# Kernel optimization log

Measured on AMD Instinct MI355X. Metric: run time of the kernel, lower is better.

## Reference

```python
import jax, jax.numpy as jnp
import numpy as np

N = 50000       # nodes
E = 800000      # edges (avg degree 16)
D_IN = 128      # input_dim
HID = 128       # hidden_dim
G_FEAT = 32     # g_feat_dim
G = 64          # number of graphs in batch
EPS = 1e-5      # BatchNorm eps


def _lin_init(key, fan_in, fan_out):
    s = 1.0 / np.sqrt(fan_in)
    return jax.random.uniform(key, (fan_in, fan_out), jnp.float32, -s, s)


def setup_inputs() -> dict:
    key = jax.random.key(0)
    ks = jax.random.split(key, 24)
    inp = {
        'x': jax.random.normal(ks[0], (N, D_IN), jnp.float32),
        'edge_index': jax.random.randint(ks[1], (2, E), 0, N, jnp.int64),
        'batch': jnp.sort(jax.random.randint(ks[2], (N,), 0, G, jnp.int64)),
        'g_feats': jax.random.normal(ks[3], (G, G_FEAT), jnp.float32),
    }
    dims = [D_IN, HID, HID]
    k = 4
    for i, din in enumerate(dims):
        inp[f'Wl{i}'] = _lin_init(ks[k], din, HID); k += 1   # lin_l (neighbors, has bias)
        inp[f'bl{i}'] = jnp.zeros((HID,), jnp.float32)
        inp[f'Wr{i}'] = _lin_init(ks[k], din, HID); k += 1   # lin_r (self, no bias in PyG)
        inp[f'gamma{i}'] = jnp.ones((HID,), jnp.float32)
        inp[f'beta{i}'] = jnp.zeros((HID,), jnp.float32)
    inp['W1'] = _lin_init(ks[k], 2 * HID + G_FEAT, HID); k += 1
    inp['b1'] = jnp.zeros((HID,), jnp.float32)
    inp['W2'] = _lin_init(ks[k], HID, HID // 2); k += 1
    inp['b2'] = jnp.zeros((HID // 2,), jnp.float32)
    inp['W3'] = _lin_init(ks[k], HID // 2, 1); k += 1
    inp['b3'] = jnp.zeros((1,), jnp.float32)
    return inp


def _sage_conv(h, src, dst, Wl, bl, Wr):
    # mean-aggregate neighbor messages x_j into target i, then lin_l(agg)+lin_r(self)
    msgs = h[src]  # [E, d] irregular gather
    agg = jax.ops.segment_sum(msgs, dst, num_segments=N)
    cnt = jax.ops.segment_sum(jnp.ones((E,), h.dtype), dst, num_segments=N)
    agg = agg / jnp.clip(cnt, 1.0)[:, None]
    return agg @ Wl + bl + h @ Wr


def _batch_norm(h, gamma, beta):
    mu = jnp.mean(h, axis=0)
    var = jnp.var(h, axis=0)
    return gamma * (h - mu) * jax.lax.rsqrt(var + EPS) + beta


def _forward(x, edge_index, batch, g_feats, convs, head):
    src, dst = edge_index[0], edge_index[1]
    h = x
    for (Wl, bl, Wr, gamma, beta) in convs:
        h = jax.nn.relu(_batch_norm(_sage_conv(h, src, dst, Wl, bl, Wr), gamma, beta))
        # dropout p=0.01: identity in eval/reference mode
    cnt = jnp.clip(jax.ops.segment_sum(jnp.ones((N,), h.dtype), batch, num_segments=G), 1.0)
    hg_mean = jax.ops.segment_sum(h, batch, num_segments=G) / cnt[:, None]
    hg_max = jax.ops.segment_max(h, batch, num_segments=G)
    W1, b1, W2, b2, W3, b3 = head
    m = jnp.concatenate([hg_mean, hg_max, g_feats], axis=1)  # [G, 2*HID+G_FEAT]
    m = jax.nn.relu(m @ W1 + b1)
    m = jax.nn.relu(m @ W2 + b2)
    return (m @ W3 + b3).reshape(-1)  # [G]


def reference(x, edge_index, batch, g_feats,
              Wl0, bl0, Wr0, gamma0, beta0,
              Wl1, bl1, Wr1, gamma1, beta1,
              Wl2, bl2, Wr2, gamma2, beta2,
              W1, b1, W2, b2, W3, b3):
    convs = [(Wl0, bl0, Wr0, gamma0, beta0),
             (Wl1, bl1, Wr1, gamma1, beta1),
             (Wl2, bl2, Wr2, gamma2, beta2)]
    head = (W1, b1, W2, b2, W3, b3)
    return _forward(x, edge_index, batch, g_feats, convs, head)
```

## Files before the change

### kernel.cpp

```cpp
#include <hip/hip_runtime.h>
#include <stdint.h>

#define NN 50000
#define NE 800000
#define HID 128
#define NG 64
#define BN_EPS 1e-5f
#define SC_NB 8
#define SC_BSZ ((NN + SC_NB - 1) / SC_NB)
#define SC_CHUNK 4096
#define SC_CHUNKS ((NE + SC_CHUNK - 1) / SC_CHUNK)
#define CAP 96
#define LAYER_BLOCKS (NN / 16)
#define NPART 64

typedef __bf16 bf16x8 __attribute__((ext_vector_type(8)));
typedef float floatx4 __attribute__((ext_vector_type(4)));

__device__ __forceinline__ float b2f(unsigned short u) {
    union { unsigned int i; float f; } x; x.i = ((unsigned int)u) << 16; return x.f;
}
__device__ __forceinline__ float blo(unsigned int d) { return __uint_as_float(d << 16); }
__device__ __forceinline__ float bhi(unsigned int d) { return __uint_as_float(d & 0xffff0000u); }
__device__ __forceinline__ unsigned short f2b(float f) {
    union { float f; unsigned int i; } x; x.f = f; unsigned int i = x.i;
    if ((i & 0x7f800000u) == 0x7f800000u) return (unsigned short)(i >> 16);
    return (unsigned short)((i + 0x7fffu + ((i >> 16) & 1u)) >> 16);
}
__device__ __forceinline__ unsigned int pack2(float f0, float f1) {
    return (((unsigned int)f2b(f1)) << 16) | f2b(f0);
}
__device__ __forceinline__ float2 bn_pair_part(const float* __restrict__ part,
                                               const float* __restrict__ gamma,
                                               const float* __restrict__ beta, int c) {
    float s = 0.f, sq = 0.f;
#pragma unroll 8
    for (int k = 0; k < NPART; ++k) {
        s += part[k * 256 + c];
        sq += part[k * 256 + 128 + c];
    }
    float mu = s * (1.f / NN);
    float var = sq * (1.f / NN) - mu * mu;
    float sc = gamma[c] * rsqrtf(var + BN_EPS);
    return make_float2(sc, beta[c] - mu * sc);
}
__device__ __forceinline__ int lbound(const int* __restrict__ batch, int val) {
    int lo = 0, hi = NN;
    while (lo < hi) { int mid = (lo + hi) >> 1; if (batch[mid] < val) lo = mid + 1; else hi = mid; }
    return lo;
}

__global__ void k_setup(const float* __restrict__ x, unsigned short* xb, int* cnt,
                        float* part, float* pool_sum, int* pool_max,
                        const float* __restrict__ Wl0, const float* __restrict__ Wr0,
                        const float* __restrict__ Wl1, const float* __restrict__ Wr1,
                        const float* __restrict__ Wl2, const float* __restrict__ Wr2,
                        unsigned short* Bp) {
    int i = blockIdx.x * 256 + threadIdx.x;
    if (i < NN * 64) {
        float2 v = ((const float2*)x)[i];
        ((unsigned int*)xb)[i] = pack2(v.x, v.y);
    }
    if (i < NN) cnt[i] = 0;
    if (i < 3 * NPART * 256) part[i] = 0.f;
    if (i < NG * HID) { pool_sum[i] = 0.f; pool_max[i] = 0; }
    if (i < 3 * 32768) {
        int layer = i >> 15;
        int r = i & 32767;
        int nt = r >> 12, kk = (r >> 9) & 7, l = (r >> 3) & 63, j = r & 7;
        int k = kk * 32 + (l >> 4) * 8 + j;
        int n = nt * 16 + (l & 15);
        const float* Wl = layer == 0 ? Wl0 : (layer == 1 ? Wl1 : Wl2);
        const float* Wr = layer == 0 ? Wr0 : (layer == 1 ? Wr1 : Wr2);
        Bp[i] = f2b((k < 128) ? Wl[k * 128 + n] : Wr[(k - 128) * 128 + n]);
    }
}

__global__ void k_scatter(const int* __restrict__ src, const int* __restrict__ dst,
                          int* cnt, int* col) {
    int bucket = blockIdx.x & (SC_NB - 1);
    int chunk = blockIdx.x / SC_NB;
    int lo = bucket * SC_BSZ, hi = lo + SC_BSZ;
    int base = chunk * SC_CHUNK;
#pragma unroll
    for (int i = 0; i < SC_CHUNK / 256; ++i) {
        int e = base + i * 256 + threadIdx.x;
        if (e < NE) {
            int d = dst[e];
            if (d >= lo && d < hi) {
                int p = atomicAdd(&cnt[d], 1);
                if (p < CAP) col[d * CAP + p] = src[e];
            }
        }
    }
}

__global__ void __launch_bounds__(256) k_layer(const unsigned short* __restrict__ h,
                                               const int* __restrict__ cnt,
                                               const int* __restrict__ col,
                                               const unsigned short* __restrict__ Bg,
                                               float* __restrict__ part,
                                               unsigned short* __restrict__ out) {
    __shared__ uint4 aggt4[256];
    __shared__ uint4 selft4[256];
    int t = threadIdx.x;
    int wid = t >> 6, lane = t & 63;
    const uint4* h4 = (const uint4*)h;
    {
        int slot = lane >> 4, sub = lane & 15;
        int nl = wid * 4 + slot;
        int node = blockIdx.x * 16 + nl;
        int n = cnt[node]; if (n > CAP) n = CAP;
        const int* row = col + (size_t)node * CAP;
        uint4 sv = h4[(size_t)node * 16 + sub];
        float a0 = 0.f, a1 = 0.f, a2 = 0.f, a3 = 0.f, a4 = 0.f, a5 = 0.f, a6 = 0.f, a7 = 0.f;
        int j = 0;
        for (; j + 8 <= n; j += 8) {
            int u0 = row[j], u1 = row[j + 1], u2 = row[j + 2], u3 = row[j + 3];
            int u4 = row[j + 4], u5 = row[j + 5], u6 = row[j + 6], u7 = row[j + 7];
            uint4 v0 = h4[(size_t)u0 * 16 + sub];
            uint4 v1 = h4[(size_t)u1 * 16 + sub];
            uint4 v2 = h4[(size_t)u2 * 16 + sub];
            uint4 v3 = h4[(size_t)u3 * 16 + sub];
            uint4 v4 = h4[(size_t)u4 * 16 + sub];
            uint4 v5 = h4[(size_t)u5 * 16 + sub];
            uint4 v6 = h4[(size_t)u6 * 16 + sub];
            uint4 v7 = h4[(size_t)u7 * 16 + sub];
            a0 += ((blo(v0.x) + blo(v1.x)) + (blo(v2.x) + blo(v3.x))) +
                  ((blo(v4.x) + blo(v5.x)) + (blo(v6.x) + blo(v7.x)));
            a1 += ((bhi(v0.x) + bhi(v1.x)) + (bhi(v2.x) + bhi(v3.x))) +
                  ((bhi(v4.x) + bhi(v5.x)) + (bhi(v6.x) + bhi(v7.x)));
            a2 += ((blo(v0.y) + blo(v1.y)) + (blo(v2.y) + blo(v3.y))) +
                  ((blo(v4.y) + blo(v5.y)) + (blo(v6.y) + blo(v7.y)));
            a3 += ((bhi(v0.y) + bhi(v1.y)) + (bhi(v2.y) + bhi(v3.y))) +
                  ((bhi(v4.y) + bhi(v5.y)) + (bhi(v6.y) + bhi(v7.y)));
            a4 += ((blo(v0.z) + blo(v1.z)) + (blo(v2.z) + blo(v3.z))) +
                  ((blo(v4.z) + blo(v5.z)) + (blo(v6.z) + blo(v7.z)));
            a5 += ((bhi(v0.z) + bhi(v1.z)) + (bhi(v2.z) + bhi(v3.z))) +
                  ((bhi(v4.z) + bhi(v5.z)) + (bhi(v6.z) + bhi(v7.z)));
            a6 += ((blo(v0.w) + blo(v1.w)) + (blo(v2.w) + blo(v3.w))) +
                  ((blo(v4.w) + blo(v5.w)) + (blo(v6.w) + blo(v7.w)));
            a7 += ((bhi(v0.w) + bhi(v1.w)) + (bhi(v2.w) + bhi(v3.w))) +
                  ((bhi(v4.w) + bhi(v5.w)) + (bhi(v6.w) + bhi(v7.w)));
        }
        for (; j + 4 <= n; j += 4) {
            int u0 = row[j], u1 = row[j + 1], u2 = row[j + 2], u3 = row[j + 3];
            uint4 v0 = h4[(size_t)u0 * 16 + sub];
            uint4 v1 = h4[(size_t)u1 * 16 + sub];
            uint4 v2 = h4[(size_t)u2 * 16 + sub];
            uint4 v3 = h4[(size_t)u3 * 16 + sub];
            a0 += (blo(v0.x) + blo(v1.x)) + (blo(v2.x) + blo(v3.x));
            a1 += (bhi(v0.x) + bhi(v1.x)) + (bhi(v2.x) + bhi(v3.x));
            a2 += (blo(v0.y) + blo(v1.y)) + (blo(v2.y) + blo(v3.y));
            a3 += (bhi(v0.y) + bhi(v1.y)) + (bhi(v2.y) + bhi(v3.y));
            a4 += (blo(v0.z) + blo(v1.z)) + (blo(v2.z) + blo(v3.z));
            a5 += (bhi(v0.z) + bhi(v1.z)) + (bhi(v2.z) + bhi(v3.z));
            a6 += (blo(v0.w) + blo(v1.w)) + (blo(v2.w) + blo(v3.w));
            a7 += (bhi(v0.w) + bhi(v1.w)) + (bhi(v2.w) + bhi(v3.w));
        }
        for (; j < n; ++j) {
            int u = row[j];
            uint4 v = h4[(size_t)u * 16 + sub];
            a0 += blo(v.x);  a1 += bhi(v.x);
            a2 += blo(v.y);  a3 += bhi(v.y);
            a4 += blo(v.z);  a5 += bhi(v.z);
            a6 += blo(v.w);  a7 += bhi(v.w);
        }
        float inv = (n > 0) ? 1.f / (float)n : 0.f;
        uint4 o;
        o.x = pack2(a0 * inv, a1 * inv);
        o.y = pack2(a2 * inv, a3 * inv);
        o.z = pack2(a4 * inv, a5 * inv);
        o.w = pack2(a6 * inv, a7 * inv);
        int swz = sub ^ (nl & 7);
        aggt4[nl * 16 + swz] = o;
        selft4[nl * 16 + swz] = sv;
    }
    __syncthreads();
    int m = lane & 15, q = lane >> 4;
    int mbase = blockIdx.x * 16;
    const bf16x8* Bv = (const bf16x8*)Bg;
    bf16x8 af[8];
#pragma unroll
    for (int kk = 0; kk < 4; ++kk) {
        int ci = (kk * 4 + q) ^ (m & 7);
        af[kk] = *(const bf16x8*)&aggt4[m * 16 + ci];
        af[4 + kk] = *(const bf16x8*)&selft4[m * 16 + ci];
    }
    floatx4 acc[2];
    acc[0] = (floatx4){0.f, 0.f, 0.f, 0.f};
    acc[1] = (floatx4){0.f, 0.f, 0.f, 0.f};
#pragma unroll
    for (int kk = 0; kk < 8; ++kk) {
#pragma unroll
        for (int ntl = 0; ntl < 2; ++ntl) {
            int nt = wid * 2 + ntl;
            bf16x8 b = Bv[(nt * 8 + kk) * 64 + lane];
            acc[ntl] = __builtin_amdgcn_mfma_f32_16x16x32_bf16(af[kk], b, acc[ntl], 0, 0, 0);
        }
    }
    float s8[2] = {0.f, 0.f}, ss8[2] = {0.f, 0.f};
#pragma unroll
    for (int ntl = 0; ntl < 2; ++ntl) {
        int c = (wid * 2 + ntl) * 16 + m;
#pragma unroll
        for (int reg = 0; reg < 4; ++reg) {
            int r = mbase + q * 4 + reg;
            float v = acc[ntl][reg];
            out[(size_t)r * 128 + c] = f2b(v);
            s8[ntl] += v;
            ss8[ntl] += v * v;
        }
        s8[ntl] += __shfl_xor(s8[ntl], 16, 64);  s8[ntl] += __shfl_xor(s8[ntl], 32, 64);
        ss8[ntl] += __shfl_xor(ss8[ntl], 16, 64); ss8[ntl] += __shfl_xor(ss8[ntl], 32, 64);
    }
    float* pb = part + (blockIdx.x & (NPART - 1)) * 256;
    if (lane < 16) {
#pragma unroll
        for (int ntl = 0; ntl < 2; ++ntl) {
            int c = (wid * 2 + ntl) * 16 + m;
            atomicAdd(&pb[c], s8[ntl]);
            atomicAdd(&pb[128 + c], ss8[ntl]);
        }
    }
}

__global__ void k_norm(const unsigned short* __restrict__ pre,
                       const float* __restrict__ part, const float* __restrict__ gamma,
                       const float* __restrict__ beta, unsigned short* __restrict__ hn) {
    __shared__ float sc[128], sh[128];
    int t = threadIdx.x;
    if (t < 128) {
        float2 p = bn_pair_part(part, gamma, beta, t);
        sc[t] = p.x; sh[t] = p.y;
    }
    __syncthreads();
#pragma unroll
    for (int ii = 0; ii < 4; ++ii) {
        int i = (blockIdx.x * 4 + ii) * 256 + t;
        if (i < NN * 16) {
            uint4 v = ((const uint4*)pre)[i];
            int cb = (i & 15) * 8;
            uint4 o;
            o.x = pack2(fmaxf(blo(v.x) * sc[cb + 0] + sh[cb + 0], 0.f),
                        fmaxf(bhi(v.x) * sc[cb + 1] + sh[cb + 1], 0.f));
            o.y = pack2(fmaxf(blo(v.y) * sc[cb + 2] + sh[cb + 2], 0.f),
                        fmaxf(bhi(v.y) * sc[cb + 3] + sh[cb + 3], 0.f));
            o.z = pack2(fmaxf(blo(v.z) * sc[cb + 4] + sh[cb + 4], 0.f),
                        fmaxf(bhi(v.z) * sc[cb + 5] + sh[cb + 5], 0.f));
            o.w = pack2(fmaxf(blo(v.w) * sc[cb + 6] + sh[cb + 6], 0.f),
                        fmaxf(bhi(v.w) * sc[cb + 7] + sh[cb + 7], 0.f));
            ((uint4*)hn)[i] = o;
        }
    }
}

__global__ void k_pool(const unsigned short* __restrict__ h, const int* __restrict__ batch,
                       const float* __restrict__ part,
                       const float* __restrict__ gamma, const float* __restrict__ beta,
                       float* pool_sum, int* pool_max) {
    int g = blockIdx.x >> 3, chunk = blockIdx.x & 7;
    int s = lbound(batch, g), e1 = lbound(batch, g + 1);
    if (s >= e1) return;
    int cnt = e1 - s;
    int per = (cnt + 7) >> 3;
    int r0 = s + chunk * per;
    int r1 = min(r0 + per, e1);
    int c = threadIdx.x & 127, half = threadIdx.x >> 7;
    float2 pr = bn_pair_part(part, gamma, beta, c);
    float sm = 0.f, mx = 0.f;
    for (int r = r0 + half; r < r1; r += 2) {
        float v = fmaxf(b2f(h[(size_t)r * 128 + c]) * pr.x + pr.y, 0.f);
        sm += v;
        mx = fmaxf(mx, v);
    }
    atomicAdd(&pool_sum[g * 128 + c], sm);
    atomicMax(&pool_max[g * 128 + c], __float_as_int(mx));
}

__global__ void __launch_bounds__(128) k_head(
    const float* __restrict__ pool_sum, const int* __restrict__ pool_max,
    const int* __restrict__ batch, const float* __restrict__ gfeats,
    const float* __restrict__ W1, const float* __restrict__ bs1,
    const float* __restrict__ W2, const float* __restrict__ bs2,
    const float* __restrict__ W3, const float* __restrict__ bs3,
    float* out) {
    __shared__ float m[288];
    __shared__ float o1[128];
    __shared__ float o2[64];
    int g = blockIdx.x, t = threadIdx.x;
    int cint = lbound(batch, g + 1) - lbound(batch, g);
    float cnt = (float)(cint < 1 ? 1 : cint);
    if (t < 128) {
        m[t] = pool_sum[g * 128 + t] / cnt;
        m[128 + t] = __int_as_float(pool_max[g * 128 + t]);
    }
    if (t < 32) m[256 + t] = gfeats[g * 32 + t];
    __syncthreads();
    float acc = bs1[t];
    for (int k = 0; k < 288; ++k) acc += m[k] * W1[k * 128 + t];
    o1[t] = fmaxf(acc, 0.f);
    __syncthreads();
    if (t < 64) {
        float a2 = bs2[t];
        for (int k = 0; k < 128; ++k) a2 += o1[k] * W2[k * 64 + t];
        o2[t] = fmaxf(a2, 0.f);
    }
    __syncthreads();
    if (t < 64) {
        float p = o2[t] * W3[t];
#pragma unroll
        for (int off = 32; off; off >>= 1) p += __shfl_down(p, off, 64);
        if (t == 0) out[g] = p + bs3[0];
    }
}

extern "C" void kernel_launch(void* const* d_in, const int* in_sizes, int n_in,
                              void* d_out, int out_size, void* d_ws, size_t ws_size,
                              hipStream_t stream) {
    const float* x = (const float*)d_in[0];
    const int* ei = (const int*)d_in[1];
    const int* batch = (const int*)d_in[2];
    const float* gfeats = (const float*)d_in[3];
    const float *Wl[3], *Wr[3], *gma[3], *bta[3];
    for (int i = 0; i < 3; ++i) {
        Wl[i] = (const float*)d_in[4 + 5 * i];
        Wr[i] = (const float*)d_in[6 + 5 * i];
        gma[i] = (const float*)d_in[7 + 5 * i];
        bta[i] = (const float*)d_in[8 + 5 * i];
    }
    const float* W1 = (const float*)d_in[19];
    const float* bs1 = (const float*)d_in[20];
    const float* W2 = (const float*)d_in[21];
    const float* bs2 = (const float*)d_in[22];
    const float* W3 = (const float*)d_in[23];
    const float* bs3 = (const float*)d_in[24];

    char* p = (char*)d_ws;
    auto alloc = [&](size_t bytes) -> char* {
        char* r = p;
        p += (bytes + 255) & ~(size_t)255;
        return r;
    };
    int* cnt = (int*)alloc(NN * 4);
    int* col = (int*)alloc((size_t)NN * CAP * 4);
    float* part = (float*)alloc(3 * NPART * 256 * 4);
    float* pool_sum = (float*)alloc(NG * HID * 4);
    int* pool_max = (int*)alloc(NG * HID * 4);
    unsigned short* Bp = (unsigned short*)alloc(3 * 32768 * 2);
    unsigned short* xb = (unsigned short*)alloc((size_t)NN * 128 * 2);
    unsigned short* b0 = (unsigned short*)alloc((size_t)NN * 128 * 2);
    unsigned short* b1 = (unsigned short*)alloc((size_t)NN * 128 * 2);
    unsigned short* hn0 = (unsigned short*)alloc((size_t)NN * 128 * 2);

    const int* srcv = ei;
    const int* dstv = ei + NE;

    k_setup<<<(NN * 64 + 255) / 256, 256, 0, stream>>>(
        x, xb, cnt, part, pool_sum, pool_max,
        Wl[0], Wr[0], Wl[1], Wr[1], Wl[2], Wr[2], Bp);
    k_scatter<<<SC_CHUNKS * SC_NB, 256, 0, stream>>>(srcv, dstv, cnt, col);

    k_layer<<<LAYER_BLOCKS, 256, 0, stream>>>(xb, cnt, col, Bp, part, b0);
    k_norm<<<(NN * 16 + 1023) / 1024, 256, 0, stream>>>(b0, part, gma[0], bta[0], hn0);
    k_layer<<<LAYER_BLOCKS, 256, 0, stream>>>(hn0, cnt, col, Bp + 32768, part + 16384, b1);
    k_norm<<<(NN * 16 + 1023) / 1024, 256, 0, stream>>>(b1, part + 16384, gma[1], bta[1], xb);
    k_layer<<<LAYER_BLOCKS, 256, 0, stream>>>(xb, cnt, col, Bp + 65536, part + 32768, b0);

    k_pool<<<NG * 8, 256, 0, stream>>>(b0, batch, part + 32768, gma[2], bta[2],
                                       pool_sum, pool_max);
    k_head<<<NG, 128, 0, stream>>>(pool_sum, pool_max, batch, gfeats,
                                   W1, bs1, W2, bs2, W3, bs3, (float*)d_out);
}
```

Measured before the change: 332.1 us.

## Split per-node edge counters by parity and fuse pooling with MLP head

The edge scatter now spreads atomics across two counters per destination node, chosen by edge parity, each with its own half of the neighbor slots. This is meant to cut contention on the per-node atomic counters. The pooling and head kernels are merged into one launch: the last block to finish, detected with a global done counter, runs the MLP head for all graphs. This removes one kernel launch but runs the whole head serially in a single block, and a node whose edges fall unevenly across the two halves now overflows at 48 slots per half instead of 96 total.

```diff
diff --git a/kernel.cpp b/kernel.cpp
--- a/kernel.cpp
+++ b/kernel.cpp
@@ -11,6 +11,7 @@
 #define SC_CHUNK 4096
 #define SC_CHUNKS ((NE + SC_CHUNK - 1) / SC_CHUNK)
 #define CAP 96
+#define SUBCAP 48
 #define LAYER_BLOCKS (NN / 16)
 #define NPART 64
 
@@ -50,8 +51,8 @@
     return lo;
 }
 
-__global__ void k_setup(const float* __restrict__ x, unsigned short* xb, int* cnt,
-                        float* part, float* pool_sum, int* pool_max,
+__global__ void k_setup(const float* __restrict__ x, unsigned short* xb, int* cnt2,
+                        float* part, float* pool_sum, int* pool_max, int* done,
                         const float* __restrict__ Wl0, const float* __restrict__ Wr0,
                         const float* __restrict__ Wl1, const float* __restrict__ Wr1,
                         const float* __restrict__ Wl2, const float* __restrict__ Wr2,
@@ -61,7 +62,8 @@
         float2 v = ((const float2*)x)[i];
         ((unsigned int*)xb)[i] = pack2(v.x, v.y);
     }
-    if (i < NN) cnt[i] = 0;
+    if (i < NN * 2) cnt2[i] = 0;
+    if (i == 0) done[0] = 0;
     if (i < 3 * NPART * 256) part[i] = 0.f;
     if (i < NG * HID) { pool_sum[i] = 0.f; pool_max[i] = 0; }
     if (i < 3 * 32768) {
@@ -77,7 +79,7 @@
 }
 
 __global__ void k_scatter(const int* __restrict__ src, const int* __restrict__ dst,
-                          int* cnt, int* col) {
+                          int* cnt2, int* col) {
     int bucket = blockIdx.x & (SC_NB - 1);
     int chunk = blockIdx.x / SC_NB;
     int lo = bucket * SC_BSZ, hi = lo + SC_BSZ;
@@ -88,15 +90,16 @@
         if (e < NE) {
             int d = dst[e];
             if (d >= lo && d < hi) {
-                int p = atomicAdd(&cnt[d], 1);
-                if (p < CAP) col[d * CAP + p] = src[e];
+                int s = e & 1;
+                int p = atomicAdd(&cnt2[d * 2 + s], 1);
+                if (p < SUBCAP) col[d * CAP + s * SUBCAP + p] = src[e];
             }
         }
     }
 }
 
 __global__ void __launch_bounds__(256) k_layer(const unsigned short* __restrict__ h,
-                                               const int* __restrict__ cnt,
+                                               const int* __restrict__ cnt2,
                                                const int* __restrict__ col,
                                                const unsigned short* __restrict__ Bg,
                                                float* __restrict__ part,
@@ -110,62 +113,69 @@
         int slot = lane >> 4, sub = lane & 15;
         int nl = wid * 4 + slot;
         int node = blockIdx.x * 16 + nl;
-        int n = cnt[node]; if (n > CAP) n = CAP;
+        int2 c2 = ((const int2*)cnt2)[node];
+        int n0 = min(c2.x, SUBCAP), n1 = min(c2.y, SUBCAP);
         const int* row = col + (size_t)node * CAP;
         uint4 sv = h4[(size_t)node * 16 + sub];
         float a0 = 0.f, a1 = 0.f, a2 = 0.f, a3 = 0.f, a4 = 0.f, a5 = 0.f, a6 = 0.f, a7 = 0.f;
-        int j = 0;
-        for (; j + 8 <= n; j += 8) {
-            int u0 = row[j], u1 = row[j + 1], u2 = row[j + 2], u3 = row[j + 3];
-            int u4 = row[j + 4], u5 = row[j + 5], u6 = row[j + 6], u7 = row[j + 7];
-            uint4 v0 = h4[(size_t)u0 * 16 + sub];
-            uint4 v1 = h4[(size_t)u1 * 16 + sub];
-            uint4 v2 = h4[(size_t)u2 * 16 + sub];
-            uint4 v3 = h4[(size_t)u3 * 16 + sub];
-            uint4 v4 = h4[(size_t)u4 * 16 + sub];
-            uint4 v5 = h4[(size_t)u5 * 16 + sub];
-            uint4 v6 = h4[(size_t)u6 * 16 + sub];
-            uint4 v7 = h4[(size_t)u7 * 16 + sub];
-            a0 += ((blo(v0.x) + blo(v1.x)) + (blo(v2.x) + blo(v3.x))) +
-                  ((blo(v4.x) + blo(v5.x)) + (blo(v6.x) + blo(v7.x)));
-            a1 += ((bhi(v0.x) + bhi(v1.x)) + (bhi(v2.x) + bhi(v3.x))) +
-                  ((bhi(v4.x) + bhi(v5.x)) + (bhi(v6.x) + bhi(v7.x)));
-            a2 += ((blo(v0.y) + blo(v1.y)) + (blo(v2.y) + blo(v3.y))) +
-                  ((blo(v4.y) + blo(v5.y)) + (blo(v6.y) + blo(v7.y)));
-            a3 += ((bhi(v0.y) + bhi(v1.y)) + (bhi(v2.y) + bhi(v3.y))) +
-                  ((bhi(v4.y) + bhi(v5.y)) + (bhi(v6.y) + bhi(v7.y)));
-            a4 += ((blo(v0.z) + blo(v1.z)) + (blo(v2.z) + blo(v3.z))) +
-                  ((blo(v4.z) + blo(v5.z)) + (blo(v6.z) + blo(v7.z)));
-            a5 += ((bhi(v0.z) + bhi(v1.z)) + (bhi(v2.z) + bhi(v3.z))) +
-                  ((bhi(v4.z) + bhi(v5.z)) + (bhi(v6.z) + bhi(v7.z)));
-            a6 += ((blo(v0.w) + blo(v1.w)) + (blo(v2.w) + blo(v3.w))) +
-                  ((blo(v4.w) + blo(v5.w)) + (blo(v6.w) + blo(v7.w)));
-            a7 += ((bhi(v0.w) + bhi(v1.w)) + (bhi(v2.w) + bhi(v3.w))) +
-                  ((bhi(v4.w) + bhi(v5.w)) + (bhi(v6.w) + bhi(v7.w)));
-        }
-        for (; j + 4 <= n; j += 4) {
-            int u0 = row[j], u1 = row[j + 1], u2 = row[j + 2], u3 = row[j + 3];
-            uint4 v0 = h4[(size_t)u0 * 16 + sub];
-            uint4 v1 = h4[(size_t)u1 * 16 + sub];
-            uint4 v2 = h4[(size_t)u2 * 16 + sub];
-            uint4 v3 = h4[(size_t)u3 * 16 + sub];
-            a0 += (blo(v0.x) + blo(v1.x)) + (blo(v2.x) + blo(v3.x));
-            a1 += (bhi(v0.x) + bhi(v1.x)) + (bhi(v2.x) + bhi(v3.x));
-            a2 += (blo(v0.y) + blo(v1.y)) + (blo(v2.y) + blo(v3.y));
-            a3 += (bhi(v0.y) + bhi(v1.y)) + (bhi(v2.y) + bhi(v3.y));
-            a4 += (blo(v0.z) + blo(v1.z)) + (blo(v2.z) + blo(v3.z));
-            a5 += (bhi(v0.z) + bhi(v1.z)) + (bhi(v2.z) + bhi(v3.z));
-            a6 += (blo(v0.w) + blo(v1.w)) + (blo(v2.w) + blo(v3.w));
-            a7 += (bhi(v0.w) + bhi(v1.w)) + (bhi(v2.w) + bhi(v3.w));
-        }
-        for (; j < n; ++j) {
-            int u = row[j];
-            uint4 v = h4[(size_t)u * 16 + sub];
-            a0 += blo(v.x);  a1 += bhi(v.x);
-            a2 += blo(v.y);  a3 += bhi(v.y);
-            a4 += blo(v.z);  a5 += bhi(v.z);
-            a6 += blo(v.w);  a7 += bhi(v.w);
-        }
+#pragma unroll
+        for (int sseg = 0; sseg < 2; ++sseg) {
+            int n = sseg ? n1 : n0;
+            const int* rw = row + sseg * SUBCAP;
+            int j = 0;
+            for (; j + 8 <= n; j += 8) {
+                int u0 = rw[j], u1 = rw[j + 1], u2 = rw[j + 2], u3 = rw[j + 3];
+                int u4 = rw[j + 4], u5 = rw[j + 5], u6 = rw[j + 6], u7 = rw[j + 7];
+                uint4 v0 = h4[(size_t)u0 * 16 + sub];
+                uint4 v1 = h4[(size_t)u1 * 16 + sub];
+                uint4 v2 = h4[(size_t)u2 * 16 + sub];
+                uint4 v3 = h4[(size_t)u3 * 16 + sub];
+                uint4 v4 = h4[(size_t)u4 * 16 + sub];
+                uint4 v5 = h4[(size_t)u5 * 16 + sub];
+                uint4 v6 = h4[(size_t)u6 * 16 + sub];
+                uint4 v7 = h4[(size_t)u7 * 16 + sub];
+                a0 += ((blo(v0.x) + blo(v1.x)) + (blo(v2.x) + blo(v3.x))) +
+                      ((blo(v4.x) + blo(v5.x)) + (blo(v6.x) + blo(v7.x)));
+                a1 += ((bhi(v0.x) + bhi(v1.x)) + (bhi(v2.x) + bhi(v3.x))) +
+                      ((bhi(v4.x) + bhi(v5.x)) + (bhi(v6.x) + bhi(v7.x)));
+                a2 += ((blo(v0.y) + blo(v1.y)) + (blo(v2.y) + blo(v3.y))) +
+                      ((blo(v4.y) + blo(v5.y)) + (blo(v6.y) + blo(v7.y)));
+                a3 += ((bhi(v0.y) + bhi(v1.y)) + (bhi(v2.y) + bhi(v3.y))) +
+                      ((bhi(v4.y) + bhi(v5.y)) + (bhi(v6.y) + bhi(v7.y)));
+                a4 += ((blo(v0.z) + blo(v1.z)) + (blo(v2.z) + blo(v3.z))) +
+                      ((blo(v4.z) + blo(v5.z)) + (blo(v6.z) + blo(v7.z)));
+                a5 += ((bhi(v0.z) + bhi(v1.z)) + (bhi(v2.z) + bhi(v3.z))) +
+                      ((bhi(v4.z) + bhi(v5.z)) + (bhi(v6.z) + bhi(v7.z)));
+                a6 += ((blo(v0.w) + blo(v1.w)) + (blo(v2.w) + blo(v3.w))) +
+                      ((blo(v4.w) + blo(v5.w)) + (blo(v6.w) + blo(v7.w)));
+                a7 += ((bhi(v0.w) + bhi(v1.w)) + (bhi(v2.w) + bhi(v3.w))) +
+                      ((bhi(v4.w) + bhi(v5.w)) + (bhi(v6.w) + bhi(v7.w)));
+            }
+            for (; j + 4 <= n; j += 4) {
+                int u0 = rw[j], u1 = rw[j + 1], u2 = rw[j + 2], u3 = rw[j + 3];
+                uint4 v0 = h4[(size_t)u0 * 16 + sub];
+                uint4 v1 = h4[(size_t)u1 * 16 + sub];
+                uint4 v2 = h4[(size_t)u2 * 16 + sub];
+                uint4 v3 = h4[(size_t)u3 * 16 + sub];
+                a0 += (blo(v0.x) + blo(v1.x)) + (blo(v2.x) + blo(v3.x));
+                a1 += (bhi(v0.x) + bhi(v1.x)) + (bhi(v2.x) + bhi(v3.x));
+                a2 += (blo(v0.y) + blo(v1.y)) + (blo(v2.y) + blo(v3.y));
+                a3 += (bhi(v0.y) + bhi(v1.y)) + (bhi(v2.y) + bhi(v3.y));
+                a4 += (blo(v0.z) + blo(v1.z)) + (blo(v2.z) + blo(v3.z));
+                a5 += (bhi(v0.z) + bhi(v1.z)) + (bhi(v2.z) + bhi(v3.z));
+                a6 += (blo(v0.w) + blo(v1.w)) + (blo(v2.w) + blo(v3.w));
+                a7 += (bhi(v0.w) + bhi(v1.w)) + (bhi(v2.w) + bhi(v3.w));
+            }
+            for (; j < n; ++j) {
+                int u = rw[j];
+                uint4 v = h4[(size_t)u * 16 + sub];
+                a0 += blo(v.x);  a1 += bhi(v.x);
+                a2 += blo(v.y);  a3 += bhi(v.y);
+                a4 += blo(v.z);  a5 += bhi(v.z);
+                a6 += blo(v.w);  a7 += bhi(v.w);
+            }
+        }
+        int n = n0 + n1;
         float inv = (n > 0) ? 1.f / (float)n : 0.f;
         uint4 o;
         o.x = pack2(a0 * inv, a1 * inv);
@@ -255,63 +265,72 @@
     }
 }
 
-__global__ void k_pool(const unsigned short* __restrict__ h, const int* __restrict__ batch,
-                       const float* __restrict__ part,
-                       const float* __restrict__ gamma, const float* __restrict__ beta,
-                       float* pool_sum, int* pool_max) {
-    int g = blockIdx.x >> 3, chunk = blockIdx.x & 7;
-    int s = lbound(batch, g), e1 = lbound(batch, g + 1);
-    if (s >= e1) return;
-    int cnt = e1 - s;
-    int per = (cnt + 7) >> 3;
-    int r0 = s + chunk * per;
-    int r1 = min(r0 + per, e1);
-    int c = threadIdx.x & 127, half = threadIdx.x >> 7;
-    float2 pr = bn_pair_part(part, gamma, beta, c);
-    float sm = 0.f, mx = 0.f;
-    for (int r = r0 + half; r < r1; r += 2) {
-        float v = fmaxf(b2f(h[(size_t)r * 128 + c]) * pr.x + pr.y, 0.f);
-        sm += v;
-        mx = fmaxf(mx, v);
-    }
-    atomicAdd(&pool_sum[g * 128 + c], sm);
-    atomicMax(&pool_max[g * 128 + c], __float_as_int(mx));
-}
-
-__global__ void __launch_bounds__(128) k_head(
-    const float* __restrict__ pool_sum, const int* __restrict__ pool_max,
-    const int* __restrict__ batch, const float* __restrict__ gfeats,
+__global__ void __launch_bounds__(256) k_pool_head(
+    const unsigned short* __restrict__ h, const int* __restrict__ batch,
+    const float* __restrict__ part,
+    const float* __restrict__ gamma, const float* __restrict__ beta,
+    float* pool_sum, int* pool_max, int* done,
+    const float* __restrict__ gfeats,
     const float* __restrict__ W1, const float* __restrict__ bs1,
     const float* __restrict__ W2, const float* __restrict__ bs2,
     const float* __restrict__ W3, const float* __restrict__ bs3,
     float* out) {
-    __shared__ float m[288];
-    __shared__ float o1[128];
-    __shared__ float o2[64];
-    int g = blockIdx.x, t = threadIdx.x;
-    int cint = lbound(batch, g + 1) - lbound(batch, g);
-    float cnt = (float)(cint < 1 ? 1 : cint);
-    if (t < 128) {
-        m[t] = pool_sum[g * 128 + t] / cnt;
-        m[128 + t] = __int_as_float(pool_max[g * 128 + t]);
-    }
-    if (t < 32) m[256 + t] = gfeats[g * 32 + t];
+    __shared__ int lastFlag;
+    __shared__ float m2[2][288];
+    __shared__ float o1s[2][128];
+    __shared__ float o2s[2][64];
+    {
+        int g = blockIdx.x >> 3, chunk = blockIdx.x & 7;
+        int s = lbound(batch, g), e1 = lbound(batch, g + 1);
+        if (s < e1) {
+            int cntg = e1 - s;
+            int per = (cntg + 7) >> 3;
+            int r0 = s + chunk * per;
+            int r1 = min(r0 + per, e1);
+            int c = threadIdx.x & 127, half = threadIdx.x >> 7;
+            float2 pr = bn_pair_part(part, gamma, beta, c);
+            float sm = 0.f, mx = 0.f;
+            for (int r = r0 + half; r < r1; r += 2) {
+                float v = fmaxf(b2f(h[(size_t)r * 128 + c]) * pr.x + pr.y, 0.f);
+                sm += v;
+                mx = fmaxf(mx, v);
+            }
+            atomicAdd(&pool_sum[g * 128 + c], sm);
+            atomicMax(&pool_max[g * 128 + c], __float_as_int(mx));
+        }
+    }
+    __threadfence();
     __syncthreads();
-    float acc = bs1[t];
-    for (int k = 0; k < 288; ++k) acc += m[k] * W1[k * 128 + t];
-    o1[t] = fmaxf(acc, 0.f);
+    if (threadIdx.x == 0) lastFlag = (atomicAdd(done, 1) == NG * 8 - 1);
     __syncthreads();
-    if (t < 64) {
-        float a2 = bs2[t];
-        for (int k = 0; k < 128; ++k) a2 += o1[k] * W2[k * 64 + t];
-        o2[t] = fmaxf(a2, 0.f);
-    }
-    __syncthreads();
-    if (t < 64) {
-        float p = o2[t] * W3[t];
-#pragma unroll
-        for (int off = 32; off; off >>= 1) p += __shfl_down(p, off, 64);
-        if (t == 0) out[g] = p + bs3[0];
+    if (!lastFlag) return;
+    __threadfence();
+    int t = threadIdx.x, half = t >> 7, tc = t & 127;
+    for (int gb = 0; gb < NG; gb += 2) {
+        int g = gb + half;
+        int cint = lbound(batch, g + 1) - lbound(batch, g);
+        float cnt = (float)(cint < 1 ? 1 : cint);
+        m2[half][tc] = pool_sum[g * 128 + tc] / cnt;
+        m2[half][128 + tc] = __int_as_float(pool_max[g * 128 + tc]);
+        if (tc < 32) m2[half][256 + tc] = gfeats[g * 32 + tc];
+        __syncthreads();
+        float acc = bs1[tc];
+        for (int k = 0; k < 288; ++k) acc += m2[half][k] * W1[k * 128 + tc];
+        o1s[half][tc] = fmaxf(acc, 0.f);
+        __syncthreads();
+        if (tc < 64) {
+            float a2 = bs2[tc];
+            for (int k = 0; k < 128; ++k) a2 += o1s[half][k] * W2[k * 64 + tc];
+            o2s[half][tc] = fmaxf(a2, 0.f);
+        }
+        __syncthreads();
+        if (tc < 64) {
+            float pz = o2s[half][tc] * W3[tc];
+#pragma unroll
+            for (int off = 32; off; off >>= 1) pz += __shfl_down(pz, off, 64);
+            if (tc == 0) out[g] = pz + bs3[0];
+        }
+        __syncthreads();
     }
 }
 
@@ -342,11 +361,12 @@
         p += (bytes + 255) & ~(size_t)255;
         return r;
     };
-    int* cnt = (int*)alloc(NN * 4);
+    int* cnt2 = (int*)alloc((size_t)NN * 2 * 4);
     int* col = (int*)alloc((size_t)NN * CAP * 4);
     float* part = (float*)alloc(3 * NPART * 256 * 4);
     float* pool_sum = (float*)alloc(NG * HID * 4);
     int* pool_max = (int*)alloc(NG * HID * 4);
+    int* done = (int*)alloc(256);
     unsigned short* Bp = (unsigned short*)alloc(3 * 32768 * 2);
     unsigned short* xb = (unsigned short*)alloc((size_t)NN * 128 * 2);
     unsigned short* b0 = (unsigned short*)alloc((size_t)NN * 128 * 2);
@@ -357,18 +377,17 @@
     const int* dstv = ei + NE;
 
     k_setup<<<(NN * 64 + 255) / 256, 256, 0, stream>>>(
-        x, xb, cnt, part, pool_sum, pool_max,
+        x, xb, cnt2, part, pool_sum, pool_max, done,
         Wl[0], Wr[0], Wl[1], Wr[1], Wl[2], Wr[2], Bp);
-    k_scatter<<<SC_CHUNKS * SC_NB, 256, 0, stream>>>(srcv, dstv, cnt, col);
-
-    k_layer<<<LAYER_BLOCKS, 256, 0, stream>>>(xb, cnt, col, Bp, part, b0);
+    k_scatter<<<SC_CHUNKS * SC_NB, 256, 0, stream>>>(srcv, dstv, cnt2, col);
+
+    k_layer<<<LAYER_BLOCKS, 256, 0, stream>>>(xb, cnt2, col, Bp, part, b0);
     k_norm<<<(NN * 16 + 1023) / 1024, 256, 0, stream>>>(b0, part, gma[0], bta[0], hn0);
-    k_layer<<<LAYER_BLOCKS, 256, 0, stream>>>(hn0, cnt, col, Bp + 32768, part + 16384, b1);
+    k_layer<<<LAYER_BLOCKS, 256, 0, stream>>>(hn0, cnt2, col, Bp + 32768, part + 16384, b1);
     k_norm<<<(NN * 16 + 1023) / 1024, 256, 0, stream>>>(b1, part + 16384, gma[1], bta[1], xb);
-    k_layer<<<LAYER_BLOCKS, 256, 0, stream>>>(xb, cnt, col, Bp + 65536, part + 32768, b0);
-
-    k_pool<<<NG * 8, 256, 0, stream>>>(b0, batch, part + 32768, gma[2], bta[2],
-                                       pool_sum, pool_max);
-    k_head<<<NG, 128, 0, stream>>>(pool_sum, pool_max, batch, gfeats,
-                                   W1, bs1, W2, bs2, W3, bs3, (float*)d_out);
-}
+    k_layer<<<LAYER_BLOCKS, 256, 0, stream>>>(xb, cnt2, col, Bp + 65536, part + 32768, b0);
+
+    k_pool_head<<<NG * 8, 256, 0, stream>>>(b0, batch, part + 32768, gma[2], bta[2],
+                                            pool_sum, pool_max, done, gfeats,
+                                            W1, bs1, W2, bs2, W3, bs3, (float*)d_out);
+}
```

Result: slower. 691.9 us (+108.4%).
